# Optimization experiments

Hardware: AMD Instinct MI355X
Metric: run time of the kernel (lower is better)

Reference implementation:

```python
import jax, jax.numpy as jnp
import numpy as np
import math

B, L, CH, H, NL, N2 = 32, 4096, 1, 256, 4, 32  # batch, seq, channels, d_model, n_layers, d_state//2
LN_EPS = 1e-5


def setup_inputs() -> dict:
    key = jax.random.key(0)
    ks = jax.random.split(key, 12)
    rn = lambda k, shape, s=1.0: (jax.random.normal(k, shape, dtype=jnp.float32) * s)
    inp = {}
    inp["x"] = rn(ks[0], (B, L, CH))
    inp["enc_w"] = rn(ks[1], (H, CH), 1.0 / math.sqrt(CH))
    inp["enc_b"] = jnp.zeros((H,), jnp.float32)
    # S4D kernel parameters, stacked over layers (standard S4D init)
    dt_min, dt_max = 1e-3, 1e-1
    u = jax.random.uniform(ks[2], (NL, H))
    inp["log_dt"] = (u * (math.log(dt_max) - math.log(dt_min)) + math.log(dt_min)).astype(jnp.float32)
    inp["log_A_real"] = jnp.full((NL, H, N2), math.log(0.5), jnp.float32)
    inp["A_imag"] = jnp.broadcast_to(math.pi * jnp.arange(N2, dtype=jnp.float32), (NL, H, N2)) + jnp.zeros((NL, H, N2), jnp.float32)
    inp["C_re"] = rn(ks[3], (NL, H, N2))
    inp["C_im"] = rn(ks[4], (NL, H, N2))
    inp["D"] = rn(ks[5], (NL, H))
    # output_linear: 1x1 Conv1d H->2H followed by GLU
    inp["glu_w"] = rn(ks[6], (NL, 2 * H, H), 1.0 / math.sqrt(H))
    inp["glu_b"] = jnp.zeros((NL, 2 * H), jnp.float32)
    inp["ln_g"] = jnp.ones((NL, H), jnp.float32)
    inp["ln_b"] = jnp.zeros((NL, H), jnp.float32)
    inp["dec1_w"] = rn(ks[7], (1, L), 1.0 / math.sqrt(L))
    inp["dec1_b"] = jnp.zeros((1,), jnp.float32)
    inp["dec2_w"] = rn(ks[8], (1, H), 1.0 / math.sqrt(H))
    inp["dec2_b"] = jnp.zeros((1,), jnp.float32)
    return inp


def _s4d_layer(u_bhl, log_dt, log_A_real, A_imag, C_re, C_im, D, glu_w, glu_b):
    """S4D block on (B, H, L): FFT conv with diagonal-SSM kernel + skip D + GELU + GLU output linear."""
    Lx = u_bhl.shape[-1]
    dt = jnp.exp(log_dt)                          # (H,)
    A = -jnp.exp(log_A_real) + 1j * A_imag        # (H, N2) complex
    C = C_re + 1j * C_im                          # (H, N2)
    dtA = A * dt[:, None]                         # (H, N2)
    Ck = C * (jnp.exp(dtA) - 1.0) / A             # ZOH-style discretized C
    # Vandermonde kernel: k[h, l] = 2 * Re( sum_n Ck[h,n] * exp(dtA[h,n] * l) )
    expdtA = jnp.exp(dtA[:, :, None] * jnp.arange(Lx, dtype=jnp.float32))  # (H, N2, L)
    k = 2.0 * jnp.einsum('hn,hnl->hl', Ck, expdtA).real                    # (H, L)
    # causal conv via zero-padded FFT
    kf = jnp.fft.rfft(k, n=2 * Lx)
    uf = jnp.fft.rfft(u_bhl, n=2 * Lx)
    y = jnp.fft.irfft(uf * kf, n=2 * Lx)[..., :Lx]
    y = y + u_bhl * D[:, None]
    y = jax.nn.gelu(y, approximate=False)
    # 1x1 conv H -> 2H, then GLU over the channel dim
    y = jnp.einsum('oh,bhl->bol', glu_w, y) + glu_b[:, None]
    a, g = jnp.split(y, 2, axis=-2)
    return a * jax.nn.sigmoid(g)


def reference(x, enc_w, enc_b, log_dt, log_A_real, A_imag, C_re, C_im, D,
              glu_w, glu_b, ln_g, ln_b, dec1_w, dec1_b, dec2_w, dec2_b):
    h = x @ enc_w.T + enc_b                 # (B, L, H)
    h = jnp.swapaxes(h, -1, -2)             # (B, H, L)
    for i in range(NL):
        z = _s4d_layer(h, log_dt[i], log_A_real[i], A_imag[i], C_re[i], C_im[i],
                       D[i], glu_w[i], glu_b[i])
        h = z + h                           # residual (dropout = identity in eval)
        ht = jnp.swapaxes(h, -1, -2)        # (B, L, H) -> LayerNorm over H (postnorm)
        mu = ht.mean(-1, keepdims=True)
        var = ht.var(-1, keepdims=True)
        ht = (ht - mu) / jnp.sqrt(var + LN_EPS) * ln_g[i] + ln_b[i]
        h = jnp.swapaxes(ht, -1, -2)
    y = jnp.einsum('bhl,ol->bho', h, dec1_w) + dec1_b   # (B, H, 1)
    y = y.squeeze(-1)                                    # (B, H)
    y = y @ dec2_w.T + dec2_b                            # (B, 1)
    y = y.squeeze(-1)                                    # (B,)
    return jax.nn.sigmoid(y)
```

## Files before the change

kernel.cpp:

```cpp
#include <hip/hip_runtime.h>
#include <math.h>

#define WS_WT   16777216
#define WS_Y1   17039360
#define WS_A256 17047552
#define WS_V    17063936
#define WS_ABUF 19161088
#define WS_S    29646848

typedef unsigned short ushort_t;
struct __attribute__((aligned(8))) us4 { ushort_t x, y, z, w; };
typedef short bf16x8 __attribute__((ext_vector_type(8)));
typedef float f32x4  __attribute__((ext_vector_type(4)));

__device__ __forceinline__ float bf2f(ushort_t u) {
    union { unsigned int i; float f; } c; c.i = ((unsigned int)u) << 16; return c.f;
}
__device__ __forceinline__ ushort_t f2bf(float f) {
    union { float f; unsigned int i; } c; c.f = f;
    unsigned int x = c.i;
    unsigned int r = (x + 0x7FFF + ((x >> 16) & 1)) >> 16;
    return (ushort_t)r;
}

__global__ __launch_bounds__(256) void enc_kernel(const float* __restrict__ x,
    const float* __restrict__ ew, const float* __restrict__ eb, ushort_t* __restrict__ Hb)
{
    int i = blockIdx.x * 256 + threadIdx.x;
    int l8 = i & 511;
    int h  = (i >> 9) & 255;
    int b  = i >> 17;
    const float* xp = x + ((size_t)b << 12) + (l8 << 3);
    float4 a0 = ((const float4*)xp)[0];
    float4 a1 = ((const float4*)xp)[1];
    float w = ew[h], bb = eb[h];
    us4 o0, o1;
    o0.x = f2bf(fmaf(a0.x, w, bb)); o0.y = f2bf(fmaf(a0.y, w, bb));
    o0.z = f2bf(fmaf(a0.z, w, bb)); o0.w = f2bf(fmaf(a0.w, w, bb));
    o1.x = f2bf(fmaf(a1.x, w, bb)); o1.y = f2bf(fmaf(a1.y, w, bb));
    o1.z = f2bf(fmaf(a1.z, w, bb)); o1.w = f2bf(fmaf(a1.w, w, bb));
    us4* op = (us4*)(Hb + ((size_t)i << 3));
    op[0] = o0; op[1] = o1;
}

__global__ __launch_bounds__(256) void wtb_kernel(const float* __restrict__ gw, ushort_t* __restrict__ wTb)
{
    int i = blockIdx.x * 256 + threadIdx.x;
    wTb[i] = f2bf(gw[i]);
}

__global__ __launch_bounds__(256) void prep_kernel(
    const float* __restrict__ log_dt, const float* __restrict__ lAr,
    const float* __restrict__ Aim_, const float* __restrict__ Cre,
    const float* __restrict__ Cim, ushort_t* __restrict__ Abuf,
    ushort_t* __restrict__ Vg, float* __restrict__ a256tab, int li)
{
    __shared__ float s_ar[32], s_ai[32], s_ckr[32], s_cki[32];
    __shared__ float powr[8][32], powi[8][32];
    __shared__ float karr[256];
    __shared__ ushort_t Vt[256][66];
    int t = threadIdx.x;
    int h = blockIdx.x;
    int pb = (li * 256 + h) * 32;

    if (t < 32) {
        int s = t;
        float dt = expf(log_dt[li * 256 + h]);
        float Are = -expf(lAr[pb + s]);
        float Ai  = Aim_[pb + s];
        float e = expf(Are * dt);
        float ar = e * cosf(Ai * dt), ai = e * sinf(Ai * dt);
        float inv = 1.f / (Are * Are + Ai * Ai);
        float numr = ar - 1.f, numi = ai;
        float tr = (numr * Are + numi * Ai) * inv;
        float ti = (numi * Are - numr * Ai) * inv;
        float cr = Cre[pb + s], ci = Cim[pb + s];
        s_ar[s] = ar; s_ai[s] = ai;
        s_ckr[s] = 2.f * (cr * tr - ci * ti);
        s_cki[s] = 2.f * (cr * ti + ci * tr);
        float xr = ar, xi = ai;
        for (int k = 0; k < 8; k++) {
            powr[k][s] = xr; powi[k][s] = xi;
            float nr = xr * xr - xi * xi;
            float ni = 2.f * xr * xi;
            xr = nr; xi = ni;
        }
        a256tab[h * 64 + s * 2] = xr;
        a256tab[h * 64 + s * 2 + 1] = xi;
    }
    __syncthreads();

    int d = t;
    float adr[32], adi[32];
    #pragma unroll
    for (int s = 0; s < 32; s++) { adr[s] = 1.f; adi[s] = 0.f; }
    #pragma unroll
    for (int bit = 0; bit < 8; bit++) {
        if (d & (1 << bit)) {
            #pragma unroll
            for (int s = 0; s < 32; s++) {
                float pr_ = powr[bit][s], pi_ = powi[bit][s];
                float nr = adr[s] * pr_ - adi[s] * pi_;
                float ni = adr[s] * pi_ + adi[s] * pr_;
                adr[s] = nr; adi[s] = ni;
            }
        }
    }
    float kd = 0.f;
    #pragma unroll
    for (int s = 0; s < 32; s++) kd += s_ckr[s] * adr[s] - s_cki[s] * adi[s];
    karr[d] = kd;
    unsigned int wrow[32];
    #pragma unroll
    for (int s = 0; s < 32; s++) {
        float wr = adr[s] * s_ar[s] - adi[s] * s_ai[s];
        float wi = adr[s] * s_ai[s] + adi[s] * s_ar[s];
        float v0 = s_ckr[s] * wr - s_cki[s] * wi;
        float v1 = -(s_ckr[s] * wi + s_cki[s] * wr);
        wrow[s] = (unsigned int)f2bf(v0) | ((unsigned int)f2bf(v1) << 16);
    }
    {
        ushort_t* arow = Abuf + (size_t)h * 81920 + (size_t)d * 320 + 256;
        #pragma unroll
        for (int q = 0; q < 8; q++) {
            uint4 v; v.x = wrow[q*4]; v.y = wrow[q*4+1]; v.z = wrow[q*4+2]; v.w = wrow[q*4+3];
            *(uint4*)(arow + q * 8) = v;
        }
    }
    {
        int e = 255 - d;
        float evr[32], evi[32];
        #pragma unroll
        for (int s = 0; s < 32; s++) { evr[s] = 1.f; evi[s] = 0.f; }
        #pragma unroll
        for (int bit = 0; bit < 8; bit++) {
            if (e & (1 << bit)) {
                #pragma unroll
                for (int s = 0; s < 32; s++) {
                    float pr_ = powr[bit][s], pi_ = powi[bit][s];
                    float nr = evr[s] * pr_ - evi[s] * pi_;
                    float ni = evr[s] * pi_ + evi[s] * pr_;
                    evr[s] = nr; evi[s] = ni;
                }
            }
        }
        #pragma unroll
        for (int s = 0; s < 32; s++) {
            Vt[d][2*s]   = f2bf(evr[s]);
            Vt[d][2*s+1] = f2bf(evi[s]);
        }
    }
    __syncthreads();

    {
        ushort_t* trow = Abuf + (size_t)h * 81920 + (size_t)t * 320;
        for (int j4 = 0; j4 < 64; j4++) {
            int j = j4 * 4;
            us4 v;
            v.x = (j     <= t) ? f2bf(karr[t - j    ]) : (ushort_t)0;
            v.y = (j + 1 <= t) ? f2bf(karr[t - j - 1]) : (ushort_t)0;
            v.z = (j + 2 <= t) ? f2bf(karr[t - j - 2]) : (ushort_t)0;
            v.w = (j + 3 <= t) ? f2bf(karr[t - j - 3]) : (ushort_t)0;
            *(us4*)(trow + j) = v;
        }
    }
    {
        int m = t >> 2, jq = t & 3;
        ushort_t* vrow = Vg + (size_t)h * 16384 + (size_t)m * 256 + jq * 64;
        for (int j4 = 0; j4 < 16; j4++) {
            int j = jq * 64 + j4 * 4;
            us4 v;
            v.x = Vt[j][m]; v.y = Vt[j+1][m]; v.z = Vt[j+2][m]; v.w = Vt[j+3][m];
            *(us4*)(vrow + j4 * 4) = v;
        }
    }
}

__global__ __launch_bounds__(256, 2) void vgemm_kernel(
    const ushort_t* __restrict__ U, const ushort_t* __restrict__ Vg,
    ushort_t* __restrict__ Sb, int b0, int ntot)
{
    __shared__ ushort_t yt[64 * 264];
    int t = threadIdx.x;
    int h = blockIdx.x;
    int tile = blockIdx.y;
    int nl = t & 63, kq = t >> 6;
    int n = tile * 64 + nl;
    const ushort_t* ub = U + (size_t)(b0 + (n >> 4)) * 1048576 + (size_t)h * 4096 + (n & 15) * 256;
    #pragma unroll
    for (int i = 0; i < 8; i++) {
        int k = kq * 64 + i * 8;
        *(uint4*)(&yt[nl * 264 + k]) = *(const uint4*)(ub + k);
    }
    __syncthreads();

    int lane = t & 63, w = t >> 6;
    int ln15 = lane & 15, quad = lane >> 4;
    const ushort_t* va = Vg + (size_t)h * 16384 + (size_t)(w * 16 + ln15) * 256;
    f32x4 acc[4] = {};
    for (int ks = 0; ks < 8; ks++) {
        int kk = ks * 32 + quad * 8;
        bf16x8 af = *(const bf16x8*)(va + kk);
        #pragma unroll
        for (int nt = 0; nt < 4; nt++) {
            bf16x8 bf_ = *(const bf16x8*)(&yt[(nt * 16 + ln15) * 264 + kk]);
            acc[nt] = __builtin_amdgcn_mfma_f32_16x16x32_bf16(af, bf_, acc[nt], 0, 0, 0);
        }
    }
    #pragma unroll
    for (int nt = 0; nt < 4; nt++) {
        int nn = tile * 64 + nt * 16 + ln15;
        ushort_t* sp = Sb + ((size_t)h * ntot + nn) * 64 + w * 16 + quad * 4;
        us4 v;
        v.x = f2bf(acc[nt][0]); v.y = f2bf(acc[nt][1]);
        v.z = f2bf(acc[nt][2]); v.w = f2bf(acc[nt][3]);
        *(us4*)sp = v;
    }
}

__global__ __launch_bounds__(256) void scan_kernel(
    ushort_t* __restrict__ Sb, const float* __restrict__ a256tab, int ntot)
{
    int t = threadIdx.x;
    int lane = t & 63;
    int w = t >> 6;
    int sub = lane >> 5, s = lane & 31;
    int r = blockIdx.x * 8 + w * 2 + sub;
    int h = r & 255, bl = r >> 8;
    float m2r = a256tab[h * 64 + s * 2], m2i = a256tab[h * 64 + s * 2 + 1];
    float sr = 0.f, si = 0.f;
    for (int c = 0; c < 16; c++) {
        unsigned int* p = (unsigned int*)Sb + ((size_t)h * ntot + bl * 16 + c) * 32 + s;
        unsigned int sv = *p;
        float Sr = bf2f((ushort_t)(sv & 0xFFFF));
        float Si = bf2f((ushort_t)(sv >> 16));
        *p = (unsigned int)f2bf(sr) | ((unsigned int)f2bf(si) << 16);
        float nsr = m2r * sr - m2i * si + Sr;
        float nsi = m2r * si + m2i * sr + Si;
        sr = nsr; si = nsi;
    }
}

__global__ __launch_bounds__(256, 2) void dgemm_kernel(
    const ushort_t* __restrict__ U, const ushort_t* __restrict__ Abuf,
    const ushort_t* __restrict__ Sb, const float* __restrict__ Dp,
    ushort_t* __restrict__ G, int li, int b0, int ntot)
{
    __shared__ ushort_t yt[64 * 328];
    int t = threadIdx.x;
    int h = blockIdx.x;
    int tile = blockIdx.y;
    int nl = t & 63, kq = t >> 6;
    int n = tile * 64 + nl;
    const ushort_t* ub = U + (size_t)(b0 + (n >> 4)) * 1048576 + (size_t)h * 4096 + (n & 15) * 256;
    #pragma unroll
    for (int i = 0; i < 8; i++) {
        int k = kq * 64 + i * 8;
        *(uint4*)(&yt[nl * 328 + k]) = *(const uint4*)(ub + k);
    }
    {
        const uint4* sp = (const uint4*)(Sb + ((size_t)h * ntot + n) * 64 + kq * 16);
        *(uint4*)(&yt[nl * 328 + 256 + kq * 16]) = sp[0];
        *(uint4*)(&yt[nl * 328 + 256 + kq * 16 + 8]) = sp[1];
    }
    __syncthreads();

    int lane = t & 63, w = t >> 6;
    int ln15 = lane & 15, quad = lane >> 4;
    const ushort_t* Ah = Abuf + (size_t)h * 81920;
    f32x4 acc[4][4] = {};
    for (int ks = 0; ks < 10; ks++) {
        int kk = ks * 32 + quad * 8;
        bf16x8 af[4];
        #pragma unroll
        for (int mt = 0; mt < 4; mt++)
            af[mt] = *(const bf16x8*)(Ah + (size_t)(w * 64 + mt * 16 + ln15) * 320 + kk);
        #pragma unroll
        for (int nt = 0; nt < 4; nt++) {
            bf16x8 bf_ = *(const bf16x8*)(&yt[(nt * 16 + ln15) * 328 + kk]);
            #pragma unroll
            for (int mt = 0; mt < 4; mt++)
                acc[mt][nt] = __builtin_amdgcn_mfma_f32_16x16x32_bf16(af[mt], bf_, acc[mt][nt], 0, 0, 0);
        }
    }
    float Dh = Dp[li * 256 + h];
    #pragma unroll
    for (int mt = 0; mt < 4; mt++) {
        #pragma unroll
        for (int nt = 0; nt < 4; nt++) {
            int nn = tile * 64 + nt * 16 + ln15;
            int lb = w * 64 + mt * 16 + quad * 4;
            us4 uv = *(const us4*)(&yt[(nt * 16 + ln15) * 328 + lb]);
            float uu[4] = {bf2f(uv.x), bf2f(uv.y), bf2f(uv.z), bf2f(uv.w)};
            us4 o;
            ushort_t* op = &o.x;
            #pragma unroll
            for (int rr = 0; rr < 4; rr++) {
                float v = acc[mt][nt][rr] + Dh * uu[rr];
                float g = v * 0.5f * (1.f + erff(v * 0.70710678118654752f));
                op[rr] = f2bf(g);
            }
            ushort_t* gp = G + ((size_t)(nn >> 4) * 256 + h) * 4096 + (nn & 15) * 256 + lb;
            *(us4*)gp = o;
        }
    }
}

#define LDK 268
__global__ __launch_bounds__(256, 2) void gluln_kernel(
    const ushort_t* __restrict__ G, const ushort_t* __restrict__ wTb,
    const float* __restrict__ glu_b, const float* __restrict__ ln_g,
    const float* __restrict__ ln_b, ushort_t* __restrict__ Hb, int li, int b0)
{
    __shared__ ushort_t yt[64 * LDK];
    __shared__ float redS[16][66], redQ[16][66];
    __shared__ float mup[64], rstd[64];
    int t = threadIdx.x;
    int pf = blockIdx.x * 64;
    int bloc = pf >> 12;
    int l0 = pf & 4095;
    int b = b0 + bloc;

    const ushort_t* gb = G + (size_t)bloc * 1048576 + l0;
    unsigned int* dst = (unsigned int*)&yt[0];
    #pragma unroll
    for (int i = 0; i < 4; i++) {
        int hp = ((i & 1) << 6) + (t >> 2);
        int pg = ((i >> 1) << 2) + (t & 3);
        int h0 = hp * 2;
        uint4 va = *(const uint4*)(gb + (size_t)h0 * 4096 + pg * 8);
        uint4 vb = *(const uint4*)(gb + (size_t)(h0 + 1) * 4096 + pg * 8);
        const ushort_t* ra = (const ushort_t*)&va;
        const ushort_t* rb = (const ushort_t*)&vb;
        #pragma unroll
        for (int j = 0; j < 8; j++) {
            unsigned int v = (unsigned int)ra[j] | ((unsigned int)rb[j] << 16);
            dst[(pg * 8 + j) * (LDK / 2) + hp] = v;
        }
    }
    __syncthreads();

    int lane = t & 63, w = t >> 6;
    int ln15 = lane & 15, quad = lane >> 4;
    int oA = w * 64;
    const ushort_t* wA = wTb + li * 131072;

    f32x4 accA[4][4] = {};
    f32x4 accG[4][4] = {};

    for (int ks = 0; ks < 8; ks++) {
        int kk = ks * 32 + quad * 8;
        bf16x8 af[4], gf[4];
        #pragma unroll
        for (int mt = 0; mt < 4; mt++) {
            int oa = oA + mt * 16 + ln15;
            af[mt] = *(const bf16x8*)(wA + (size_t)oa * 256 + kk);
            gf[mt] = *(const bf16x8*)(wA + (size_t)(oa + 256) * 256 + kk);
        }
        bf16x8 bfr[4];
        #pragma unroll
        for (int nt = 0; nt < 4; nt++) {
            const us4* yp = (const us4*)&yt[(nt * 16 + ln15) * LDK + kk];
            us4 lo = yp[0], hi = yp[1];
            bf16x8 v;
            v[0] = (short)lo.x; v[1] = (short)lo.y; v[2] = (short)lo.z; v[3] = (short)lo.w;
            v[4] = (short)hi.x; v[5] = (short)hi.y; v[6] = (short)hi.z; v[7] = (short)hi.w;
            bfr[nt] = v;
        }
        #pragma unroll
        for (int mt = 0; mt < 4; mt++)
            #pragma unroll
            for (int nt = 0; nt < 4; nt++) {
                accA[mt][nt] = __builtin_amdgcn_mfma_f32_16x16x32_bf16(af[mt], bfr[nt], accA[mt][nt], 0, 0, 0);
                accG[mt][nt] = __builtin_amdgcn_mfma_f32_16x16x32_bf16(gf[mt], bfr[nt], accG[mt][nt], 0, 0, 0);
            }
    }

    ushort_t* hb_ = Hb + (size_t)b * 1048576;
    float ps[4] = {0.f, 0.f, 0.f, 0.f}, pq[4] = {0.f, 0.f, 0.f, 0.f};
    #pragma unroll
    for (int mt = 0; mt < 4; mt++) {
        #pragma unroll
        for (int r = 0; r < 4; r++) {
            int o = oA + mt * 16 + quad * 4 + r;
            float ba = glu_b[li * 512 + o];
            float bg = glu_b[li * 512 + 256 + o];
            const ushort_t* hrow = hb_ + (size_t)o * 4096 + l0 + ln15;
            #pragma unroll
            for (int nt = 0; nt < 4; nt++) {
                float a = accA[mt][nt][r] + ba;
                float g = accG[mt][nt][r] + bg;
                float z = a / (1.f + expf(-g));
                float hn = z + bf2f(hrow[nt * 16]);
                accA[mt][nt][r] = hn;
                ps[nt] += hn; pq[nt] = fmaf(hn, hn, pq[nt]);
            }
        }
    }
    int slot = w * 4 + quad;
    #pragma unroll
    for (int nt = 0; nt < 4; nt++) {
        redS[slot][nt * 16 + ln15] = ps[nt];
        redQ[slot][nt * 16 + ln15] = pq[nt];
    }
    __syncthreads();
    if (t < 64) {
        float S = 0.f, Q = 0.f;
        #pragma unroll
        for (int s_ = 0; s_ < 16; s_++) { S += redS[s_][t]; Q += redQ[s_][t]; }
        float mu = S * (1.f / 256.f);
        float var = Q * (1.f / 256.f) - mu * mu;
        mup[t] = mu; rstd[t] = rsqrtf(var + 1e-5f);
    }
    __syncthreads();
    #pragma unroll
    for (int mt = 0; mt < 4; mt++) {
        #pragma unroll
        for (int r = 0; r < 4; r++) {
            int o = oA + mt * 16 + quad * 4 + r;
            float gm = ln_g[li * 256 + o];
            float bt = ln_b[li * 256 + o];
            ushort_t* hrow = hb_ + (size_t)o * 4096 + l0 + ln15;
            #pragma unroll
            for (int nt = 0; nt < 4; nt++) {
                int p = nt * 16 + ln15;
                float v = (accA[mt][nt][r] - mup[p]) * rstd[p] * gm + bt;
                hrow[nt * 16] = f2bf(v);
            }
        }
    }
}

__global__ __launch_bounds__(256) void dec1_kernel(const ushort_t* __restrict__ Hb,
    const float* __restrict__ w1, const float* __restrict__ b1, float* __restrict__ y1)
{
    int bh = blockIdx.x;
    const ushort_t* base = Hb + (size_t)bh * 4096;
    int t = threadIdx.x;
    float s = 0.f;
    for (int l = t; l < 4096; l += 256) s = fmaf(bf2f(base[l]), w1[l], s);
    #pragma unroll
    for (int d = 32; d > 0; d >>= 1) s += __shfl_xor(s, d, 64);
    __shared__ float red[4];
    if ((t & 63) == 0) red[t >> 6] = s;
    __syncthreads();
    if (t == 0) y1[bh] = red[0] + red[1] + red[2] + red[3] + b1[0];
}

__global__ __launch_bounds__(256) void dec2_kernel(const float* __restrict__ y1,
    const float* __restrict__ w2, const float* __restrict__ b2, float* __restrict__ out)
{
    int t = threadIdx.x;
    int b = blockIdx.x * 4 + (t >> 6);
    int lane = t & 63;
    float s = 0.f;
    #pragma unroll
    for (int k = 0; k < 4; k++) s = fmaf(y1[b * 256 + lane + k * 64], w2[lane + k * 64], s);
    #pragma unroll
    for (int d = 32; d > 0; d >>= 1) s += __shfl_xor(s, d, 64);
    if (lane == 0) out[b] = 1.f / (1.f + expf(-(s + b2[0])));
}

extern "C" void kernel_launch(void* const* d_in, const int* in_sizes, int n_in,
                              void* d_out, int out_size, void* d_ws, size_t ws_size,
                              hipStream_t stream)
{
    const float* x      = (const float*)d_in[0];
    const float* enc_w  = (const float*)d_in[1];
    const float* enc_b  = (const float*)d_in[2];
    const float* log_dt = (const float*)d_in[3];
    const float* lAr    = (const float*)d_in[4];
    const float* Aim    = (const float*)d_in[5];
    const float* Cre    = (const float*)d_in[6];
    const float* Cim    = (const float*)d_in[7];
    const float* Dp     = (const float*)d_in[8];
    const float* glu_w  = (const float*)d_in[9];
    const float* glu_b  = (const float*)d_in[10];
    const float* ln_g   = (const float*)d_in[11];
    const float* ln_b   = (const float*)d_in[12];
    const float* w1     = (const float*)d_in[13];
    const float* b1     = (const float*)d_in[14];
    const float* w2     = (const float*)d_in[15];
    const float* b2     = (const float*)d_in[16];

    float* ws = (float*)d_ws;
    ushort_t* Hb   = (ushort_t*)ws;
    ushort_t* wTb  = (ushort_t*)(ws + WS_WT);
    float* y1      = ws + WS_Y1;
    float* a256    = ws + WS_A256;
    ushort_t* Vg   = (ushort_t*)(ws + WS_V);
    ushort_t* Abuf = (ushort_t*)(ws + WS_ABUF);
    float* outp    = (float*)d_out;

    size_t wsf = ws_size / 4;
    int nb = 32;
    while (nb > 4 && (size_t)WS_S + (size_t)nb * 655360 > wsf) nb >>= 1;
    int ntot = nb * 16;
    ushort_t* Sb = (ushort_t*)(ws + WS_S);
    ushort_t* Gb = (ushort_t*)(ws + WS_S + (size_t)nb * 131072);

    wtb_kernel<<<2048, 256, 0, stream>>>(glu_w, wTb);
    enc_kernel<<<16384, 256, 0, stream>>>(x, enc_w, enc_b, Hb);
    for (int li = 0; li < 4; li++) {
        prep_kernel<<<256, 256, 0, stream>>>(log_dt, lAr, Aim, Cre, Cim, Abuf, Vg, a256, li);
        for (int b0 = 0; b0 < 32; b0 += nb) {
            vgemm_kernel<<<dim3(256, nb / 4), 256, 0, stream>>>(Hb, Vg, Sb, b0, ntot);
            scan_kernel<<<nb * 32, 256, 0, stream>>>(Sb, a256, ntot);
            dgemm_kernel<<<dim3(256, nb / 4), 256, 0, stream>>>(Hb, Abuf, Sb, Dp, Gb, li, b0, ntot);
            gluln_kernel<<<nb * 64, 256, 0, stream>>>(Gb, wTb, glu_b, ln_g, ln_b, Hb, li, b0);
        }
    }
    dec1_kernel<<<8192, 256, 0, stream>>>(Hb, w1, b1, y1);
    dec2_kernel<<<8, 256, 0, stream>>>(y1, w2, b2, outp);
}
```

Baseline: 1.132 ms.

## Swizzle LDS tiles in vgemm/dgemm and transpose GLU MFMA for vectorized epilogue

Replaces the padded LDS rows in vgemm and dgemm with an XOR-swizzled 16-byte chunk layout, so bank conflicts are avoided without padding and LDS use shrinks. In gluln, the MFMA operands are swapped so each lane holds four consecutive sequence positions for one channel. That lets the residual loads and LayerNorm stores use 8-byte vector accesses instead of scalar strided ones. The LayerNorm statistics are now reduced with wave shuffles before a smaller shared-memory reduction, which adds shuffle instructions and more live registers.

```diff
diff --git a/kernel.cpp b/kernel.cpp
--- a/kernel.cpp
+++ b/kernel.cpp
@@ -180,7 +180,7 @@
     const ushort_t* __restrict__ U, const ushort_t* __restrict__ Vg,
     ushort_t* __restrict__ Sb, int b0, int ntot)
 {
-    __shared__ ushort_t yt[64 * 264];
+    __shared__ ushort_t yt[64 * 256];
     int t = threadIdx.x;
     int h = blockIdx.x;
     int tile = blockIdx.y;
@@ -189,8 +189,8 @@
     const ushort_t* ub = U + (size_t)(b0 + (n >> 4)) * 1048576 + (size_t)h * 4096 + (n & 15) * 256;
     #pragma unroll
     for (int i = 0; i < 8; i++) {
-        int k = kq * 64 + i * 8;
-        *(uint4*)(&yt[nl * 264 + k]) = *(const uint4*)(ub + k);
+        int c = kq * 8 + i;
+        *(uint4*)(&yt[nl * 256 + ((c ^ (nl & 7)) << 3)]) = *(const uint4*)(ub + c * 8);
     }
     __syncthreads();
 
@@ -199,11 +199,11 @@
     const ushort_t* va = Vg + (size_t)h * 16384 + (size_t)(w * 16 + ln15) * 256;
     f32x4 acc[4] = {};
     for (int ks = 0; ks < 8; ks++) {
-        int kk = ks * 32 + quad * 8;
-        bf16x8 af = *(const bf16x8*)(va + kk);
+        int c = ks * 4 + quad;
+        bf16x8 af = *(const bf16x8*)(va + ks * 32 + quad * 8);
         #pragma unroll
         for (int nt = 0; nt < 4; nt++) {
-            bf16x8 bf_ = *(const bf16x8*)(&yt[(nt * 16 + ln15) * 264 + kk]);
+            bf16x8 bf_ = *(const bf16x8*)(&yt[(nt * 16 + ln15) * 256 + ((c ^ (ln15 & 7)) << 3)]);
             acc[nt] = __builtin_amdgcn_mfma_f32_16x16x32_bf16(af, bf_, acc[nt], 0, 0, 0);
         }
     }
@@ -246,38 +246,42 @@
     const ushort_t* __restrict__ Sb, const float* __restrict__ Dp,
     ushort_t* __restrict__ G, int li, int b0, int ntot)
 {
-    __shared__ ushort_t yt[64 * 328];
+    __shared__ ushort_t yt[64 * 320];
     int t = threadIdx.x;
     int h = blockIdx.x;
     int tile = blockIdx.y;
     int nl = t & 63, kq = t >> 6;
     int n = tile * 64 + nl;
+    int sw = nl & 7;
     const ushort_t* ub = U + (size_t)(b0 + (n >> 4)) * 1048576 + (size_t)h * 4096 + (n & 15) * 256;
     #pragma unroll
     for (int i = 0; i < 8; i++) {
-        int k = kq * 64 + i * 8;
-        *(uint4*)(&yt[nl * 328 + k]) = *(const uint4*)(ub + k);
+        int c = kq * 8 + i;
+        *(uint4*)(&yt[nl * 320 + ((c ^ sw) << 3)]) = *(const uint4*)(ub + c * 8);
     }
     {
         const uint4* sp = (const uint4*)(Sb + ((size_t)h * ntot + n) * 64 + kq * 16);
-        *(uint4*)(&yt[nl * 328 + 256 + kq * 16]) = sp[0];
-        *(uint4*)(&yt[nl * 328 + 256 + kq * 16 + 8]) = sp[1];
+        int c0 = 32 + kq * 2;
+        *(uint4*)(&yt[nl * 320 + ((c0 ^ sw) << 3)]) = sp[0];
+        *(uint4*)(&yt[nl * 320 + (((c0 + 1) ^ sw) << 3)]) = sp[1];
     }
     __syncthreads();
 
     int lane = t & 63, w = t >> 6;
     int ln15 = lane & 15, quad = lane >> 4;
+    int rsw = ln15 & 7;
     const ushort_t* Ah = Abuf + (size_t)h * 81920;
     f32x4 acc[4][4] = {};
     for (int ks = 0; ks < 10; ks++) {
         int kk = ks * 32 + quad * 8;
+        int c = ks * 4 + quad;
         bf16x8 af[4];
         #pragma unroll
         for (int mt = 0; mt < 4; mt++)
             af[mt] = *(const bf16x8*)(Ah + (size_t)(w * 64 + mt * 16 + ln15) * 320 + kk);
         #pragma unroll
         for (int nt = 0; nt < 4; nt++) {
-            bf16x8 bf_ = *(const bf16x8*)(&yt[(nt * 16 + ln15) * 328 + kk]);
+            bf16x8 bf_ = *(const bf16x8*)(&yt[(nt * 16 + ln15) * 320 + ((c ^ rsw) << 3)]);
             #pragma unroll
             for (int mt = 0; mt < 4; mt++)
                 acc[mt][nt] = __builtin_amdgcn_mfma_f32_16x16x32_bf16(af[mt], bf_, acc[mt][nt], 0, 0, 0);
@@ -290,7 +294,8 @@
         for (int nt = 0; nt < 4; nt++) {
             int nn = tile * 64 + nt * 16 + ln15;
             int lb = w * 64 + mt * 16 + quad * 4;
-            us4 uv = *(const us4*)(&yt[(nt * 16 + ln15) * 328 + lb]);
+            int c = lb >> 3, co = lb & 7;
+            us4 uv = *(const us4*)(&yt[(nt * 16 + ln15) * 320 + ((c ^ rsw) << 3) + co]);
             float uu[4] = {bf2f(uv.x), bf2f(uv.y), bf2f(uv.z), bf2f(uv.w)};
             us4 o;
             ushort_t* op = &o.x;
@@ -313,7 +318,7 @@
     const float* __restrict__ ln_b, ushort_t* __restrict__ Hb, int li, int b0)
 {
     __shared__ ushort_t yt[64 * LDK];
-    __shared__ float redS[16][66], redQ[16][66];
+    __shared__ float sred[4][64], sqred[4][64];
     __shared__ float mup[64], rstd[64];
     int t = threadIdx.x;
     int pf = blockIdx.x * 64;
@@ -371,62 +376,94 @@
         for (int mt = 0; mt < 4; mt++)
             #pragma unroll
             for (int nt = 0; nt < 4; nt++) {
-                accA[mt][nt] = __builtin_amdgcn_mfma_f32_16x16x32_bf16(af[mt], bfr[nt], accA[mt][nt], 0, 0, 0);
-                accG[mt][nt] = __builtin_amdgcn_mfma_f32_16x16x32_bf16(gf[mt], bfr[nt], accG[mt][nt], 0, 0, 0);
+                accA[mt][nt] = __builtin_amdgcn_mfma_f32_16x16x32_bf16(bfr[nt], af[mt], accA[mt][nt], 0, 0, 0);
+                accG[mt][nt] = __builtin_amdgcn_mfma_f32_16x16x32_bf16(bfr[nt], gf[mt], accG[mt][nt], 0, 0, 0);
             }
     }
 
     ushort_t* hb_ = Hb + (size_t)b * 1048576;
-    float ps[4] = {0.f, 0.f, 0.f, 0.f}, pq[4] = {0.f, 0.f, 0.f, 0.f};
+    us4 hold[4][4];
     #pragma unroll
     for (int mt = 0; mt < 4; mt++) {
+        const ushort_t* hrow = hb_ + (size_t)(oA + mt * 16 + ln15) * 4096 + l0 + quad * 4;
+        #pragma unroll
+        for (int nt = 0; nt < 4; nt++)
+            hold[mt][nt] = *(const us4*)(hrow + nt * 16);
+    }
+
+    float ba[4], bg[4];
+    #pragma unroll
+    for (int mt = 0; mt < 4; mt++) {
+        int o = oA + mt * 16 + ln15;
+        ba[mt] = glu_b[li * 512 + o];
+        bg[mt] = glu_b[li * 512 + 256 + o];
+    }
+
+    float psl[4][4] = {}, pql[4][4] = {};
+    #pragma unroll
+    for (int mt = 0; mt < 4; mt++) {
+        #pragma unroll
+        for (int nt = 0; nt < 4; nt++) {
+            const ushort_t* hp4 = &hold[mt][nt].x;
+            #pragma unroll
+            for (int r = 0; r < 4; r++) {
+                float a = accA[mt][nt][r] + ba[mt];
+                float g = accG[mt][nt][r] + bg[mt];
+                float z = a / (1.f + expf(-g));
+                float hn = z + bf2f(hp4[r]);
+                accA[mt][nt][r] = hn;
+                psl[nt][r] += hn; pql[nt][r] = fmaf(hn, hn, pql[nt][r]);
+            }
+        }
+    }
+    #pragma unroll
+    for (int nt = 0; nt < 4; nt++)
         #pragma unroll
         for (int r = 0; r < 4; r++) {
-            int o = oA + mt * 16 + quad * 4 + r;
-            float ba = glu_b[li * 512 + o];
-            float bg = glu_b[li * 512 + 256 + o];
-            const ushort_t* hrow = hb_ + (size_t)o * 4096 + l0 + ln15;
-            #pragma unroll
-            for (int nt = 0; nt < 4; nt++) {
-                float a = accA[mt][nt][r] + ba;
-                float g = accG[mt][nt][r] + bg;
-                float z = a / (1.f + expf(-g));
-                float hn = z + bf2f(hrow[nt * 16]);
-                accA[mt][nt][r] = hn;
-                ps[nt] += hn; pq[nt] = fmaf(hn, hn, pq[nt]);
-            }
-        }
-    }
-    int slot = w * 4 + quad;
-    #pragma unroll
-    for (int nt = 0; nt < 4; nt++) {
-        redS[slot][nt * 16 + ln15] = ps[nt];
-        redQ[slot][nt * 16 + ln15] = pq[nt];
+            float s = psl[nt][r], q = pql[nt][r];
+            s += __shfl_xor(s, 1, 64); q += __shfl_xor(q, 1, 64);
+            s += __shfl_xor(s, 2, 64); q += __shfl_xor(q, 2, 64);
+            s += __shfl_xor(s, 4, 64); q += __shfl_xor(q, 4, 64);
+            s += __shfl_xor(s, 8, 64); q += __shfl_xor(q, 8, 64);
+            psl[nt][r] = s; pql[nt][r] = q;
+        }
+    if (ln15 == 0) {
+        #pragma unroll
+        for (int nt = 0; nt < 4; nt++)
+            #pragma unroll
+            for (int r = 0; r < 4; r++) {
+                int p = nt * 16 + quad * 4 + r;
+                sred[w][p] = psl[nt][r];
+                sqred[w][p] = pql[nt][r];
+            }
     }
     __syncthreads();
     if (t < 64) {
-        float S = 0.f, Q = 0.f;
-        #pragma unroll
-        for (int s_ = 0; s_ < 16; s_++) { S += redS[s_][t]; Q += redQ[s_][t]; }
+        float S = (sred[0][t] + sred[1][t]) + (sred[2][t] + sred[3][t]);
+        float Q = (sqred[0][t] + sqred[1][t]) + (sqred[2][t] + sqred[3][t]);
         float mu = S * (1.f / 256.f);
         float var = Q * (1.f / 256.f) - mu * mu;
         mup[t] = mu; rstd[t] = rsqrtf(var + 1e-5f);
     }
     __syncthreads();
+
     #pragma unroll
     for (int mt = 0; mt < 4; mt++) {
-        #pragma unroll
-        for (int r = 0; r < 4; r++) {
-            int o = oA + mt * 16 + quad * 4 + r;
-            float gm = ln_g[li * 256 + o];
-            float bt = ln_b[li * 256 + o];
-            ushort_t* hrow = hb_ + (size_t)o * 4096 + l0 + ln15;
-            #pragma unroll
-            for (int nt = 0; nt < 4; nt++) {
-                int p = nt * 16 + ln15;
+        int o = oA + mt * 16 + ln15;
+        float gm = ln_g[li * 256 + o];
+        float bt = ln_b[li * 256 + o];
+        ushort_t* hrow = hb_ + (size_t)o * 4096 + l0 + quad * 4;
+        #pragma unroll
+        for (int nt = 0; nt < 4; nt++) {
+            us4 ov;
+            ushort_t* op = &ov.x;
+            #pragma unroll
+            for (int r = 0; r < 4; r++) {
+                int p = nt * 16 + quad * 4 + r;
                 float v = (accA[mt][nt][r] - mup[p]) * rstd[p] * gm + bt;
-                hrow[nt * 16] = f2bf(v);
-            }
+                op[r] = f2bf(v);
+            }
+            *(us4*)(hrow + nt * 16) = ov;
         }
     }
 }
```

Measured after the change: 1.158 ms. 1.02x slower.
